# Performance work log

Measured on AMD Instinct MI355X. Metric: run time of the kernel, lower is better.

The kernel has to match this reference:

```python
import jax, jax.numpy as jnp
import numpy as np

C = 256
RATE_CHOICE = [32, 64, 96, 128, 160, 192, 224, 256]
RATE_NUM = len(RATE_CHOICE)
MAX_RATE = max(RATE_CHOICE)
B, H, W = 16, 16, 16


def setup_inputs() -> dict:
    key = jax.random.key(0)
    k_x, k_idx, k_w = jax.random.split(key, 3)
    x = jax.random.normal(k_x, (B, C, H, W), dtype=jnp.float32)
    indexes = jax.random.randint(k_idx, (B * H * W,), 0, RATE_NUM, dtype=jnp.int64)
    # xavier_normal over (fan_in=C*MAX_RATE? torch 3D: fan_in=C*MAX_RATE, fan_out=RATE_NUM*MAX_RATE) -> use gain std
    std = float(np.sqrt(2.0 / (C + MAX_RATE)))
    weight = jax.random.normal(k_w, (RATE_NUM, C, MAX_RATE), dtype=jnp.float32) * std
    bias = jnp.zeros((RATE_NUM, MAX_RATE), dtype=jnp.float32)
    rate_choice_tensor = jnp.asarray(RATE_CHOICE, dtype=jnp.int32)
    return {"x": x, "indexes": indexes, "weight": weight, "bias": bias,
            "rate_choice_tensor": rate_choice_tensor}


def reference(x, indexes, weight, bias, rate_choice_tensor):
    Bv, Cv, Hv, Wv = x.shape
    L = Hv * Wv
    R = weight.shape[-1]
    # x: [B,C,H,W] -> [B,L,C]
    x_blc = x.reshape(Bv, Cv, L).transpose(0, 2, 1)
    # per-token gathered weights/bias
    w = weight[indexes].reshape(Bv, L, Cv, R)      # [B,L,C,R]
    b = bias[indexes].reshape(Bv, L, R)            # [B,L,R]
    # rate mask: arange(R) < rate_choice[idx]
    rc = rate_choice_tensor[indexes].reshape(Bv, L, 1)
    mask = (jnp.arange(R, dtype=rc.dtype)[None, None, :] < rc).astype(x.dtype)  # [B,L,R]
    # batched per-token matvec + bias, then mask
    y = (jnp.einsum('blc,blcr->blr', x_blc, w) + b) * mask
    x_masked = y.reshape(Bv, Hv, Wv, R).transpose(0, 3, 1, 2)     # [B,R,H,W]
    mask_bchw = mask.reshape(Bv, Hv, Wv, R).transpose(0, 3, 1, 2)
    return (x_masked, mask_bchw)
```

## Files before the change

### kernel.cpp

```cpp
#include <hip/hip_runtime.h>

#define WS_CNT    0
#define WS_BUCKET 8192
#define WS_WT     (1 << 20)
#define WS_XT     (2 << 20)
#define WS_YT     (6 << 20)
#define WS_NEED   (10 << 20)

typedef short v8s __attribute__((ext_vector_type(8)));
typedef float v4f __attribute__((ext_vector_type(4)));

__device__ __forceinline__ unsigned short bf16_rne(float f) {
  unsigned int u = __float_as_uint(f);
  return (unsigned short)((u + 0x7fffu + ((u >> 16) & 1u)) >> 16);
}
__device__ __forceinline__ float bf16_to_f(unsigned short h) {
  return __uint_as_float(((unsigned int)h) << 16);
}

__global__ __launch_bounds__(256) void prep_kernel(const float* __restrict__ x,
                                                   const int* __restrict__ idx,
                                                   const float* __restrict__ W,
                                                   int* __restrict__ cnt,
                                                   int* __restrict__ bucket2,
                                                   short* __restrict__ Wt,
                                                   float* __restrict__ xT) {
  const int bid = blockIdx.x;
  const int tid = threadIdx.x;

  if (bid < 1024) {
    __shared__ float tile[32][33];
    const int b = bid >> 6;
    const int c0 = ((bid & 63) >> 3) << 5;
    const int l0 = (bid & 7) << 5;
    const int j = tid & 31;
    const int i = tid >> 5;
#pragma unroll
    for (int ii = 0; ii < 4; ++ii)
      tile[(ii << 3) + i][j] = x[(b << 16) + ((c0 + (ii << 3) + i) << 8) + l0 + j];
    __syncthreads();
#pragma unroll
    for (int ii = 0; ii < 4; ++ii)
      xT[(((b << 8) + l0 + (ii << 3) + i) << 8) + c0 + j] = tile[j][(ii << 3) + i];
  } else if (bid < 1536) {
    __shared__ short ts[32][33];
    const int tau = bid - 1024;
    const int gg = tau >> 6;
    const int ti = tau & 63;
    const int c0 = (ti >> 3) << 5;
    const int r0 = (ti & 7) << 5;
    const int j = tid & 31, i = tid >> 5;
#pragma unroll
    for (int ii = 0; ii < 4; ++ii) {
      const int ci = (ii << 3) + i;
      ts[ci][j] = (short)bf16_rne(W[(gg << 16) + ((c0 + ci) << 8) + r0 + j]);
    }
    __syncthreads();
    const int p = tid & 15, q = tid >> 4;
#pragma unroll
    for (int rr = 0; rr < 2; ++rr) {
      const int rj = (rr << 4) + q;
      const unsigned int val =
          (unsigned int)(unsigned short)ts[(p << 1)][rj] |
          ((unsigned int)(unsigned short)ts[(p << 1) + 1][rj] << 16);
      *(unsigned int*)(Wt + (gg << 16) + ((r0 + rj) << 8) + c0 + (p << 1)) = val;
    }
  } else {
    __shared__ int lcount[8];
    const int b = bid - 1536;
    if (tid < 8) lcount[tid] = 0;
    __syncthreads();
    const int t = (b << 8) + tid;
    const int g = idx[t];
    const int p = atomicAdd(&lcount[g], 1);
    bucket2[(((b << 3) + g) << 8) + p] = t;
    __syncthreads();
    if (tid < 8) cnt[(b << 3) + tid] = lcount[tid];
  }
}

__global__ __launch_bounds__(256) void gemm_kernel(const float* __restrict__ xT,
                                                   const short* __restrict__ Wt,
                                                   const float* __restrict__ bias,
                                                   const int* __restrict__ cnt,
                                                   const int* __restrict__ bucket2,
                                                   float* __restrict__ yT) {
  const int g = blockIdx.x;
  const int tid = threadIdx.x;

  int n = 0;
#pragma unroll
  for (int b2 = 0; b2 < 16; ++b2) n += cnt[(b2 << 3) + g];
  const int t0 = blockIdx.y << 4;
  if (t0 >= n) return;
  const int ntv = min(16, n - t0);

  __shared__ int toks[16];
  __shared__ __align__(16) short As[2][16][264];

  if (tid < 16) {
    const int sl = min(t0 + tid, n - 1);
    int acc = 0, bsel = 0, off = 0;
#pragma unroll
    for (int b2 = 0; b2 < 16; ++b2) {
      const int c2 = cnt[(b2 << 3) + g];
      if (sl >= acc && sl < acc + c2) { bsel = b2; off = sl - acc; }
      acc += c2;
    }
    toks[tid] = bucket2[(((bsel << 3) + g) << 8) + off];
  }
  __syncthreads();

  {
    const int tk = tid >> 4, sub = tid & 15;
    const float* src = xT + (toks[tk] << 8) + (sub << 2);
#pragma unroll
    for (int q = 0; q < 4; ++q) {
      const float4 v = *reinterpret_cast<const float4*>(src + (q << 6));
      const int c = (sub << 2) + (q << 6);
      const unsigned short h0 = bf16_rne(v.x), h1 = bf16_rne(v.y);
      const unsigned short h2 = bf16_rne(v.z), h3 = bf16_rne(v.w);
      const unsigned short e0 = bf16_rne(v.x - bf16_to_f(h0));
      const unsigned short e1 = bf16_rne(v.y - bf16_to_f(h1));
      const unsigned short e2 = bf16_rne(v.z - bf16_to_f(h2));
      const unsigned short e3 = bf16_rne(v.w - bf16_to_f(h3));
      uint2 ph, pl;
      ph.x = (unsigned int)h0 | ((unsigned int)h1 << 16);
      ph.y = (unsigned int)h2 | ((unsigned int)h3 << 16);
      pl.x = (unsigned int)e0 | ((unsigned int)e1 << 16);
      pl.y = (unsigned int)e2 | ((unsigned int)e3 << 16);
      *reinterpret_cast<uint2*>(&As[0][tk][c]) = ph;
      *reinterpret_cast<uint2*>(&As[1][tk][c]) = pl;
    }
  }
  __syncthreads();

  const int lane = tid & 63, wid = tid >> 6;
  const int nr = (blockIdx.z << 7) + (wid << 5);
  const int li = lane & 15, quad = lane >> 4;
  const short* Bg = Wt + (g << 16);

  v4f acc[2];
#pragma unroll
  for (int nt = 0; nt < 2; ++nt) {
    const float bv = bias[(g << 8) + nr + (nt << 4) + li];
    acc[nt] = (v4f){bv, bv, bv, bv};
  }

  v8s bfr[2][2];
#pragma unroll
  for (int nt = 0; nt < 2; ++nt)
    bfr[0][nt] = *reinterpret_cast<const v8s*>(Bg + ((nr + (nt << 4) + li) << 8) + (quad << 3));

#pragma unroll
  for (int ks = 0; ks < 8; ++ks) {
    const v8s ah = *reinterpret_cast<const v8s*>(&As[0][li][(ks << 5) + (quad << 3)]);
    const v8s al = *reinterpret_cast<const v8s*>(&As[1][li][(ks << 5) + (quad << 3)]);
    v8s* bc = bfr[ks & 1];
    v8s* bn = bfr[(ks & 1) ^ 1];
    if (ks < 7) {
#pragma unroll
      for (int nt = 0; nt < 2; ++nt)
        bn[nt] = *reinterpret_cast<const v8s*>(
            Bg + ((nr + (nt << 4) + li) << 8) + ((ks + 1) << 5) + (quad << 3));
    }
#pragma unroll
    for (int nt = 0; nt < 2; ++nt) {
      acc[nt] = __builtin_amdgcn_mfma_f32_16x16x32_bf16(ah, bc[nt], acc[nt], 0, 0, 0);
      acc[nt] = __builtin_amdgcn_mfma_f32_16x16x32_bf16(al, bc[nt], acc[nt], 0, 0, 0);
    }
  }

#pragma unroll
  for (int nt = 0; nt < 2; ++nt) {
    const int nn = nr + (nt << 4) + li;
#pragma unroll
    for (int reg = 0; reg < 4; ++reg) {
      const int m = (quad << 2) + reg;
      if (m < ntv) yT[(toks[m] << 8) + nn] = acc[nt][reg];
    }
  }
}

__global__ __launch_bounds__(256) void out_kernel(const float* __restrict__ yT,
                                                  const int* __restrict__ idx,
                                                  const int* __restrict__ rate,
                                                  float* __restrict__ out) {
  __shared__ float tile[32][33];
  __shared__ int rcl[32];
  const int b = blockIdx.x;
  const int r0 = (blockIdx.y >> 3) << 5;
  const int l0 = (blockIdx.y & 7) << 5;
  const int j = threadIdx.x & 31;
  const int i = threadIdx.x >> 5;
#pragma unroll
  for (int ii = 0; ii < 4; ++ii) {
    const int l = l0 + (ii << 3) + i;
    tile[(ii << 3) + i][j] = yT[(((b << 8) + l) << 8) + r0 + j];
  }
  if (threadIdx.x < 32) rcl[threadIdx.x] = rate[idx[(b << 8) + l0 + threadIdx.x]];
  __syncthreads();
#pragma unroll
  for (int ii = 0; ii < 4; ++ii) {
    const int r = r0 + (ii << 3) + i;
    const float m = (r < rcl[j]) ? 1.0f : 0.0f;
    const int o = (b << 16) + (r << 8) + l0 + j;
    out[o] = tile[j][(ii << 3) + i] * m;
    out[(1 << 20) + o] = m;
  }
}

__global__ __launch_bounds__(256) void rate_tok_kernel(
    const float* __restrict__ x, const int* __restrict__ indexes,
    const float* __restrict__ W, const float* __restrict__ bias,
    const int* __restrict__ rate, float* __restrict__ out) {
  const int t = blockIdx.x;
  const int b = t >> 8;
  const int l = t & 255;
  const int r = threadIdx.x;
  __shared__ float xs[256];
  xs[r] = x[(b << 16) + (r << 8) + l];
  const int g = indexes[t];
  const int rc = rate[g];
  __syncthreads();
  const float* w = W + (g << 16) + r;
  float acc = bias[(g << 8) + r];
#pragma unroll 8
  for (int c = 0; c < 256; ++c) acc += xs[c] * w[c << 8];
  const float m = (r < rc) ? 1.0f : 0.0f;
  const int o = (b << 16) + (r << 8) + l;
  out[o] = acc * m;
  out[(1 << 20) + o] = m;
}

extern "C" void kernel_launch(void* const* d_in, const int* in_sizes, int n_in,
                              void* d_out, int out_size, void* d_ws, size_t ws_size,
                              hipStream_t stream) {
  const float* x    = (const float*)d_in[0];
  const int*   idx  = (const int*)d_in[1];
  const float* W    = (const float*)d_in[2];
  const float* bias = (const float*)d_in[3];
  const int*   rate = (const int*)d_in[4];
  float* out = (float*)d_out;
  char*  ws  = (char*)d_ws;

  if (ws_size >= (size_t)WS_NEED) {
    int*   cnt     = (int*)(ws + WS_CNT);
    int*   bucket2 = (int*)(ws + WS_BUCKET);
    short* Wt      = (short*)(ws + WS_WT);
    float* xT      = (float*)(ws + WS_XT);
    float* yT      = (float*)(ws + WS_YT);
    prep_kernel<<<dim3(1552), dim3(256), 0, stream>>>(x, idx, W, cnt, bucket2, Wt, xT);
    gemm_kernel<<<dim3(8, 48, 2), dim3(256), 0, stream>>>(xT, Wt, bias, cnt, bucket2, yT);
    out_kernel<<<dim3(16, 64), dim3(256), 0, stream>>>(yT, idx, rate, out);
  } else {
    rate_tok_kernel<<<dim3(4096), dim3(256), 0, stream>>>(x, idx, W, bias, rate, out);
  }
}
```

Measured before the change: 80.18 us.

## Presplit x into bf16 hi/lo in prep, write mask early, simplify gemm tiling

The bf16 hi/lo split of x now happens in the prep transpose instead of in every gemm block, so the gemm loads A fragments directly from global memory without LDS staging. The mask output is written by extra blocks in prep, and the rate mask is applied to y inside the gemm, which shrinks out_kernel to a plain transpose. The gemm now has each wave compute one 16-column tile with grid z doubled to 4, trading B-fragment reuse and prefetch for more parallel blocks. The gemm reads A straight from global with 16-byte loads per lane, which may be less efficient than the old LDS reads.

```diff
diff --git a/kernel.cpp b/kernel.cpp
--- a/kernel.cpp
+++ b/kernel.cpp
@@ -3,7 +3,8 @@
 #define WS_CNT    0
 #define WS_BUCKET 8192
 #define WS_WT     (1 << 20)
-#define WS_XT     (2 << 20)
+#define WS_XH     (2 << 20)
+#define WS_XL     (4 << 20)
 #define WS_YT     (6 << 20)
 #define WS_NEED   (10 << 20)
 
@@ -21,10 +22,13 @@
 __global__ __launch_bounds__(256) void prep_kernel(const float* __restrict__ x,
                                                    const int* __restrict__ idx,
                                                    const float* __restrict__ W,
+                                                   const int* __restrict__ rate,
                                                    int* __restrict__ cnt,
                                                    int* __restrict__ bucket2,
                                                    short* __restrict__ Wt,
-                                                   float* __restrict__ xT) {
+                                                   short* __restrict__ xbfH,
+                                                   short* __restrict__ xbfL,
+                                                   float* __restrict__ out) {
   const int bid = blockIdx.x;
   const int tid = threadIdx.x;
 
@@ -40,8 +44,14 @@
       tile[(ii << 3) + i][j] = x[(b << 16) + ((c0 + (ii << 3) + i) << 8) + l0 + j];
     __syncthreads();
 #pragma unroll
-    for (int ii = 0; ii < 4; ++ii)
-      xT[(((b << 8) + l0 + (ii << 3) + i) << 8) + c0 + j] = tile[j][(ii << 3) + i];
+    for (int ii = 0; ii < 4; ++ii) {
+      const float v = tile[j][(ii << 3) + i];
+      const unsigned short h = bf16_rne(v);
+      const unsigned short e = bf16_rne(v - bf16_to_f(h));
+      const int o = (((b << 8) + l0 + (ii << 3) + i) << 8) + c0 + j;
+      xbfH[o] = (short)h;
+      xbfL[o] = (short)e;
+    }
   } else if (bid < 1536) {
     __shared__ short ts[32][33];
     const int tau = bid - 1024;
@@ -65,7 +75,7 @@
           ((unsigned int)(unsigned short)ts[(p << 1) + 1][rj] << 16);
       *(unsigned int*)(Wt + (gg << 16) + ((r0 + rj) << 8) + c0 + (p << 1)) = val;
     }
-  } else {
+  } else if (bid < 1552) {
     __shared__ int lcount[8];
     const int b = bid - 1536;
     if (tid < 8) lcount[tid] = 0;
@@ -76,12 +86,26 @@
     bucket2[(((b << 3) + g) << 8) + p] = t;
     __syncthreads();
     if (tid < 8) cnt[(b << 3) + tid] = lcount[tid];
-  }
-}
-
-__global__ __launch_bounds__(256) void gemm_kernel(const float* __restrict__ xT,
+  } else {
+    const int v = ((bid - 1552) << 10) + (tid << 2);
+    const int b = v >> 16;
+    const int r = (v >> 8) & 255;
+    const int l = v & 255;
+    const int4 iv = *reinterpret_cast<const int4*>(idx + (b << 8) + l);
+    float4 m;
+    m.x = (r < rate[iv.x]) ? 1.0f : 0.0f;
+    m.y = (r < rate[iv.y]) ? 1.0f : 0.0f;
+    m.z = (r < rate[iv.z]) ? 1.0f : 0.0f;
+    m.w = (r < rate[iv.w]) ? 1.0f : 0.0f;
+    *reinterpret_cast<float4*>(out + (1 << 20) + v) = m;
+  }
+}
+
+__global__ __launch_bounds__(256) void gemm_kernel(const short* __restrict__ xbfH,
+                                                   const short* __restrict__ xbfL,
                                                    const short* __restrict__ Wt,
                                                    const float* __restrict__ bias,
+                                                   const int* __restrict__ rate,
                                                    const int* __restrict__ cnt,
                                                    const int* __restrict__ bucket2,
                                                    float* __restrict__ yT) {
@@ -94,10 +118,9 @@
   const int t0 = blockIdx.y << 4;
   if (t0 >= n) return;
   const int ntv = min(16, n - t0);
+  const int rc = rate[g];
 
   __shared__ int toks[16];
-  __shared__ __align__(16) short As[2][16][264];
-
   if (tid < 16) {
     const int sl = min(t0 + tid, n - 1);
     int acc = 0, bsel = 0, off = 0;
@@ -111,83 +134,37 @@
   }
   __syncthreads();
 
-  {
-    const int tk = tid >> 4, sub = tid & 15;
-    const float* src = xT + (toks[tk] << 8) + (sub << 2);
-#pragma unroll
-    for (int q = 0; q < 4; ++q) {
-      const float4 v = *reinterpret_cast<const float4*>(src + (q << 6));
-      const int c = (sub << 2) + (q << 6);
-      const unsigned short h0 = bf16_rne(v.x), h1 = bf16_rne(v.y);
-      const unsigned short h2 = bf16_rne(v.z), h3 = bf16_rne(v.w);
-      const unsigned short e0 = bf16_rne(v.x - bf16_to_f(h0));
-      const unsigned short e1 = bf16_rne(v.y - bf16_to_f(h1));
-      const unsigned short e2 = bf16_rne(v.z - bf16_to_f(h2));
-      const unsigned short e3 = bf16_rne(v.w - bf16_to_f(h3));
-      uint2 ph, pl;
-      ph.x = (unsigned int)h0 | ((unsigned int)h1 << 16);
-      ph.y = (unsigned int)h2 | ((unsigned int)h3 << 16);
-      pl.x = (unsigned int)e0 | ((unsigned int)e1 << 16);
-      pl.y = (unsigned int)e2 | ((unsigned int)e3 << 16);
-      *reinterpret_cast<uint2*>(&As[0][tk][c]) = ph;
-      *reinterpret_cast<uint2*>(&As[1][tk][c]) = pl;
-    }
-  }
-  __syncthreads();
-
   const int lane = tid & 63, wid = tid >> 6;
-  const int nr = (blockIdx.z << 7) + (wid << 5);
   const int li = lane & 15, quad = lane >> 4;
-  const short* Bg = Wt + (g << 16);
-
-  v4f acc[2];
-#pragma unroll
-  for (int nt = 0; nt < 2; ++nt) {
-    const float bv = bias[(g << 8) + nr + (nt << 4) + li];
-    acc[nt] = (v4f){bv, bv, bv, bv};
-  }
-
-  v8s bfr[2][2];
-#pragma unroll
-  for (int nt = 0; nt < 2; ++nt)
-    bfr[0][nt] = *reinterpret_cast<const v8s*>(Bg + ((nr + (nt << 4) + li) << 8) + (quad << 3));
+  const int nn = (blockIdx.z << 6) + (wid << 4) + li;
+  const short* Ah = xbfH + (toks[li] << 8);
+  const short* Al = xbfL + (toks[li] << 8);
+  const short* Bn = Wt + (g << 16) + (nn << 8);
+
+  const float bv = bias[(g << 8) + nn];
+  v4f acc = (v4f){bv, bv, bv, bv};
 
 #pragma unroll
   for (int ks = 0; ks < 8; ++ks) {
-    const v8s ah = *reinterpret_cast<const v8s*>(&As[0][li][(ks << 5) + (quad << 3)]);
-    const v8s al = *reinterpret_cast<const v8s*>(&As[1][li][(ks << 5) + (quad << 3)]);
-    v8s* bc = bfr[ks & 1];
-    v8s* bn = bfr[(ks & 1) ^ 1];
-    if (ks < 7) {
-#pragma unroll
-      for (int nt = 0; nt < 2; ++nt)
-        bn[nt] = *reinterpret_cast<const v8s*>(
-            Bg + ((nr + (nt << 4) + li) << 8) + ((ks + 1) << 5) + (quad << 3));
-    }
-#pragma unroll
-    for (int nt = 0; nt < 2; ++nt) {
-      acc[nt] = __builtin_amdgcn_mfma_f32_16x16x32_bf16(ah, bc[nt], acc[nt], 0, 0, 0);
-      acc[nt] = __builtin_amdgcn_mfma_f32_16x16x32_bf16(al, bc[nt], acc[nt], 0, 0, 0);
-    }
-  }
-
-#pragma unroll
-  for (int nt = 0; nt < 2; ++nt) {
-    const int nn = nr + (nt << 4) + li;
-#pragma unroll
-    for (int reg = 0; reg < 4; ++reg) {
-      const int m = (quad << 2) + reg;
-      if (m < ntv) yT[(toks[m] << 8) + nn] = acc[nt][reg];
-    }
+    const int ko = (ks << 5) + (quad << 3);
+    const v8s ah = *reinterpret_cast<const v8s*>(Ah + ko);
+    const v8s al = *reinterpret_cast<const v8s*>(Al + ko);
+    const v8s bb = *reinterpret_cast<const v8s*>(Bn + ko);
+    acc = __builtin_amdgcn_mfma_f32_16x16x32_bf16(ah, bb, acc, 0, 0, 0);
+    acc = __builtin_amdgcn_mfma_f32_16x16x32_bf16(al, bb, acc, 0, 0, 0);
+  }
+
+  const float m = (nn < rc) ? 1.0f : 0.0f;
+#pragma unroll
+  for (int reg = 0; reg < 4; ++reg) {
+    const int mm = (quad << 2) + reg;
+    if (mm < ntv) yT[(toks[mm] << 8) + nn] = acc[reg] * m;
   }
 }
 
 __global__ __launch_bounds__(256) void out_kernel(const float* __restrict__ yT,
-                                                  const int* __restrict__ idx,
-                                                  const int* __restrict__ rate,
                                                   float* __restrict__ out) {
   __shared__ float tile[32][33];
-  __shared__ int rcl[32];
   const int b = blockIdx.x;
   const int r0 = (blockIdx.y >> 3) << 5;
   const int l0 = (blockIdx.y & 7) << 5;
@@ -198,15 +175,11 @@
     const int l = l0 + (ii << 3) + i;
     tile[(ii << 3) + i][j] = yT[(((b << 8) + l) << 8) + r0 + j];
   }
-  if (threadIdx.x < 32) rcl[threadIdx.x] = rate[idx[(b << 8) + l0 + threadIdx.x]];
   __syncthreads();
 #pragma unroll
   for (int ii = 0; ii < 4; ++ii) {
     const int r = r0 + (ii << 3) + i;
-    const float m = (r < rcl[j]) ? 1.0f : 0.0f;
-    const int o = (b << 16) + (r << 8) + l0 + j;
-    out[o] = tile[j][(ii << 3) + i] * m;
-    out[(1 << 20) + o] = m;
+    out[(b << 16) + (r << 8) + l0 + j] = tile[j][(ii << 3) + i];
   }
 }
 
@@ -248,11 +221,14 @@
     int*   cnt     = (int*)(ws + WS_CNT);
     int*   bucket2 = (int*)(ws + WS_BUCKET);
     short* Wt      = (short*)(ws + WS_WT);
-    float* xT      = (float*)(ws + WS_XT);
+    short* xbfH    = (short*)(ws + WS_XH);
+    short* xbfL    = (short*)(ws + WS_XL);
     float* yT      = (float*)(ws + WS_YT);
-    prep_kernel<<<dim3(1552), dim3(256), 0, stream>>>(x, idx, W, cnt, bucket2, Wt, xT);
-    gemm_kernel<<<dim3(8, 48, 2), dim3(256), 0, stream>>>(xT, Wt, bias, cnt, bucket2, yT);
-    out_kernel<<<dim3(16, 64), dim3(256), 0, stream>>>(yT, idx, rate, out);
+    prep_kernel<<<dim3(2576), dim3(256), 0, stream>>>(
+        x, idx, W, rate, cnt, bucket2, Wt, xbfH, xbfL, out);
+    gemm_kernel<<<dim3(8, 48, 4), dim3(256), 0, stream>>>(
+        xbfH, xbfL, Wt, bias, rate, cnt, bucket2, yT);
+    out_kernel<<<dim3(16, 64), dim3(256), 0, stream>>>(yT, out);
   } else {
     rate_tok_kernel<<<dim3(4096), dim3(256), 0, stream>>>(x, idx, W, bias, rate, out);
   }
```

After: 89.68 us. 1.12x slower.
